# Kernel optimization log

Hardware: AMD Instinct MI355X
Metric: run time of the kernel (lower is better)

## Reference

```python
import jax, jax.numpy as jnp
import numpy as np

INPUT_DIM = 1024
OUTPUT_DIM = 1024
DEGREE = 8


def pentanacci_basis(x, degree):
    # x: [B, I] (already sigmoided). Returns [B, I, degree+1].
    # P0 = 0, P1 = 1, P2 = x, P3 = x, P4 = x^2,
    # Pn = x*P(n-1) + P(n-2) + P(n-3) + P(n-4) + P(n-5) for n >= 5
    zeros = jnp.zeros_like(x)
    ones = jnp.ones_like(x)
    seeds = [zeros, ones, x, x, x * x]
    basis = seeds[: degree + 1]
    for n in range(5, degree + 1):
        basis.append(x * basis[n - 1] + basis[n - 2] + basis[n - 3]
                     + basis[n - 4] + basis[n - 5])
    return jnp.stack(basis, axis=-1)


def setup_inputs() -> dict:
    key = jax.random.key(0)
    kx, kw = jax.random.split(key)
    x = jax.random.normal(kx, (4096, INPUT_DIM), dtype=jnp.float32)
    std = 1.0 / (INPUT_DIM * (DEGREE + 1))
    coeffs = std * jax.random.normal(kw, (INPUT_DIM, OUTPUT_DIM, DEGREE + 1),
                                     dtype=jnp.float32)
    return {"x": x, "coeffs": coeffs}


def reference(x, coeffs):
    degree = coeffs.shape[-1] - 1
    xs = jax.nn.sigmoid(x)                      # [B, I]
    basis = pentanacci_basis(xs, degree)        # [B, I, D+1]
    y = jnp.einsum('bid,iod->bo', basis, coeffs)  # [B, O]
    return y
```

## Files before the change

### kernel.cpp

```cpp
#include <hip/hip_runtime.h>
#include <stdint.h>

#define M_DIM 4096
#define I_DIM 1024
#define O_DIM 1024
#define KB 6
#define K_DIM (I_DIM * KB)
#define SPLITS 4

typedef __attribute__((ext_vector_type(8))) short short8;
typedef __attribute__((ext_vector_type(4))) float f32x4;
typedef __attribute__((ext_vector_type(4))) unsigned int u32x4;
typedef __attribute__((ext_vector_type(4))) float hfloat4;
typedef __attribute__((ext_vector_type(8))) _Float16 h16x8;

__device__ __forceinline__ unsigned short f2bf(float f) {
  union { float f; unsigned int u; } v; v.f = f;
  unsigned int u = v.u;
  unsigned int r = (u + 0x7FFFu + ((u >> 16) & 1u)) >> 16;
  return (unsigned short)r;
}

__global__ __launch_bounds__(256) void k_prep(const float* __restrict__ x,
                                              const float* __restrict__ C,
                                              unsigned short* __restrict__ A,
                                              unsigned short* __restrict__ Bt,
                                              float* __restrict__ partB) {
  const int bid = blockIdx.x;
  if (bid < 2048) {
    int t = bid * 256 + threadIdx.x;
    long e0 = (long)t * 8;
    const hfloat4* xp = (const hfloat4*)(x + e0);
    hfloat4 v0 = xp[0], v1 = xp[1];
    float xv[8];
    xv[0]=v0[0]; xv[1]=v0[1]; xv[2]=v0[2]; xv[3]=v0[3];
    xv[4]=v1[0]; xv[5]=v1[1]; xv[6]=v1[2]; xv[7]=v1[3];
    unsigned short outv[48];
#pragma unroll
    for (int e = 0; e < 8; ++e) {
      float s  = 1.0f / (1.0f + __expf(-xv[e]));
      float b2 = s, b3 = s, b4 = s * s;
      float b5 = fmaf(s, b4, b3 + b2 + 1.0f);
      float b6 = fmaf(s, b5, b4 + b3 + b2 + 1.0f);
      float b7 = fmaf(s, b6, b5 + b4 + b3 + b2);
      float b8 = fmaf(s, b7, b6 + b5 + b4 + b3);
      outv[e*6+0] = f2bf(s);
      outv[e*6+1] = f2bf(b4);
      outv[e*6+2] = f2bf(b5);
      outv[e*6+3] = f2bf(b6);
      outv[e*6+4] = f2bf(b7);
      outv[e*6+5] = f2bf(b8);
    }
    u32x4* dst = (u32x4*)(A + e0 * KB);
    const u32x4* srcv = (const u32x4*)outv;
#pragma unroll
    for (int q = 0; q < 6; ++q) dst[q] = srcv[q];
  } else {
    __shared__ unsigned short tile[32 * 192];
    __shared__ float bred[256];
    int b = bid - 2048;
    int i0 = (b & 31) * 32, o0 = (b >> 5) * 32;
    int t = threadIdx.x;
    int ol = t & 31, ig = t >> 5;
    float bsum = 0.f;
#pragma unroll
    for (int r = 0; r < 4; ++r) {
      int il = ig + r * 8;
      const float* p = C + (size_t)(i0 + il) * (O_DIM * 9) + (size_t)(o0 + ol) * 9;
      float c1 = p[1];
      float c2 = p[2], c3 = p[3], c4 = p[4], c5 = p[5], c6 = p[6], c7 = p[7], c8 = p[8];
      bsum += c1;
      unsigned short* q = &tile[ol * 192 + il * 6];
      q[0] = f2bf(c2 + c3);
      q[1] = f2bf(c4);
      q[2] = f2bf(c5);
      q[3] = f2bf(c6);
      q[4] = f2bf(c7);
      q[5] = f2bf(c8);
    }
    bred[t] = bsum;
    __syncthreads();
    if (t < 32) {
      float s = 0.f;
#pragma unroll
      for (int g = 0; g < 8; ++g) s += bred[g * 32 + t];
      partB[(size_t)(b & 31) * O_DIM + o0 + t] = s;
    }
    const u32x4* lsrc = (const u32x4*)tile;
#pragma unroll
    for (int r = 0; r < 3; ++r) {
      int c = t + r * 256;
      int row = c / 24, off = c % 24;
      u32x4* gdst = (u32x4*)(Bt + (size_t)(o0 + row) * K_DIM + (size_t)i0 * 6 + off * 8);
      *gdst = lsrc[c];
    }
  }
}

__global__ __launch_bounds__(256) void k_bias2(const float* __restrict__ partB,
                                               float* __restrict__ bias) {
  int o = blockIdx.x * 256 + threadIdx.x;
  float s = 0.f;
#pragma unroll
  for (int ib = 0; ib < 32; ++ib) s += partB[(size_t)ib * O_DIM + o];
  bias[o] = s;
}

#define SBAR __builtin_amdgcn_sched_barrier(0)

template<bool SPLIT>
__global__ __launch_bounds__(512, 2) void k_gemm8(const unsigned short* __restrict__ A,
                                                  const unsigned short* __restrict__ B,
                                                  const float* __restrict__ bias,
                                                  void* __restrict__ dst) {
  constexpr int CK = SPLIT ? (K_DIM / SPLITS) : K_DIM;
  constexpr int NT = CK / 64;
  constexpr int PPX = SPLIT ? 8 : 2;
  __shared__ char lds[131072];
  const int tid = threadIdx.x;
  const int lane = tid & 63, wid = tid >> 6;
  const int wm = wid >> 2, wn = wid & 3;
  const int l15 = lane & 15, lk = lane >> 4, l7 = lane & 7;
  const int flat = blockIdx.x + (blockIdx.y << 2) + (blockIdx.z << 6);
  const int xcd = flat & 7, slot = flat >> 3;
  const int panel = xcd * PPX + (slot >> 2);
  const int xn = slot & 3;
  const int ym = panel & 15, zk = panel >> 4;
  const int m0 = ym * 256, n0 = xn * 256;
  const size_t kb = (size_t)zk * CK;
  const int srow = tid >> 3;
  const int cg8 = (((tid & 7) ^ ((tid >> 3) & 7)) * 8);
  const int cx0 = (lk ^ l7) * 16;
  const int cx1 = ((4 + lk) ^ l7) * 16;
  const int arow = wm * 128 + l15;
  const int brow = wn * 64 + l15;

  auto gload = [&](const unsigned short* s, int ldsoff) {
    __builtin_amdgcn_global_load_lds((const __attribute__((address_space(1))) void*)s,
        (__attribute__((address_space(3))) void*)(lds + ldsoff), 16, 0, 0);
  };
  auto stageA = [&](int buf, int h, int kt2) {
    const unsigned short* s = A + (size_t)(m0 + h * 128 + srow) * K_DIM + kb + (size_t)kt2 * 64 + cg8;
    int d = buf * 65536 + h * 16384 + tid * 16;
    gload(s, d);
    gload(s + (size_t)64 * K_DIM, d + 8192);
  };
  auto stageB = [&](int buf, int h, int kt2) {
    const unsigned short* s = B + (size_t)(n0 + h * 128 + srow) * K_DIM + kb + (size_t)kt2 * 64 + cg8;
    int d = buf * 65536 + 32768 + h * 16384 + tid * 16;
    gload(s, d);
    gload(s + (size_t)64 * K_DIM, d + 8192);
  };

  short8 a0[8], b0v[4], a1[8], b1v[4];
  f32x4 acc[8][4];
#pragma unroll
  for (int i = 0; i < 8; ++i)
#pragma unroll
    for (int n = 0; n < 4; ++n)
#pragma unroll
      for (int j = 0; j < 4; ++j) acc[i][n][j] = 0.f;

  auto readK = [&](int buf, int cx, short8 (&av)[8], short8 (&bv)[4]) {
#pragma unroll
    for (int mi = 0; mi < 8; ++mi)
      av[mi] = *(const short8*)(lds + buf * 65536 + (arow + mi * 16) * 128 + cx);
#pragma unroll
    for (int ni = 0; ni < 4; ++ni)
      bv[ni] = *(const short8*)(lds + buf * 65536 + 32768 + (brow + ni * 16) * 128 + cx);
  };
  auto quadK = [&](short8 (&av)[8], short8 (&bv)[4]) {
#pragma unroll
    for (int mi = 0; mi < 8; ++mi)
#pragma unroll
      for (int ni = 0; ni < 4; ++ni)
        acc[mi][ni] = __builtin_amdgcn_mfma_f32_16x16x32_bf16(av[mi], bv[ni], acc[mi][ni], 0, 0, 0);
  };

  stageA(0, 0, 0); stageA(0, 1, 0); stageB(0, 0, 0); stageB(0, 1, 0);
  asm volatile("s_waitcnt vmcnt(0)" ::: "memory"); SBAR;
  __builtin_amdgcn_s_barrier(); SBAR;
  readK(0, cx0, a0, b0v);

#pragma unroll 1
  for (int kt = 0; kt < NT; ++kt) {
    const int buf = kt & 1, nb = buf ^ 1;
    if (kt + 1 < NT) {
      stageA(nb, 0, kt + 1); stageA(nb, 1, kt + 1);
      stageB(nb, 0, kt + 1); stageB(nb, 1, kt + 1);
    }
    readK(buf, cx1, a1, b1v);
    __builtin_amdgcn_s_setprio(1);
    quadK(a0, b0v);
    __builtin_amdgcn_s_setprio(0); SBAR;
    asm volatile("s_waitcnt lgkmcnt(0)" ::: "memory"); SBAR;
    if (kt + 1 < NT) {
      asm volatile("s_waitcnt vmcnt(0)" ::: "memory"); SBAR;
      __builtin_amdgcn_s_barrier(); SBAR;
      readK(nb, cx0, a0, b0v);
    }
    __builtin_amdgcn_s_setprio(1);
    quadK(a1, b1v);
    __builtin_amdgcn_s_setprio(0); SBAR;
  }

  if (SPLIT) {
    _Float16* base = (_Float16*)dst + (size_t)zk * ((size_t)M_DIM * O_DIM);
#pragma unroll
    for (int mi = 0; mi < 8; ++mi) {
      int r0 = m0 + wm * 128 + mi * 16 + (lk << 2);
#pragma unroll
      for (int ni = 0; ni < 4; ++ni) {
        int col = n0 + wn * 64 + ni * 16 + l15;
#pragma unroll
        for (int j = 0; j < 4; ++j)
          base[(size_t)(r0 + j) * O_DIM + col] = (_Float16)acc[mi][ni][j];
      }
    }
  } else {
    float* base = (float*)dst;
#pragma unroll
    for (int mi = 0; mi < 8; ++mi) {
      int r0 = m0 + wm * 128 + mi * 16 + (lk << 2);
#pragma unroll
      for (int ni = 0; ni < 4; ++ni) {
        int col = n0 + wn * 64 + ni * 16 + l15;
        float bv = bias[col];
#pragma unroll
        for (int j = 0; j < 4; ++j)
          base[(size_t)(r0 + j) * O_DIM + col] = acc[mi][ni][j] + bv;
      }
    }
  }
}

__global__ __launch_bounds__(256) void k_reduce(const _Float16* __restrict__ part,
                                                const float* __restrict__ bias,
                                                float* __restrict__ out) {
  size_t t = (size_t)blockIdx.x * 256 + threadIdx.x;
  size_t idx = t * 8;
  const size_t P = (size_t)M_DIM * O_DIM;
  h16x8 s0 = *(const h16x8*)(part + idx);
  h16x8 s1 = *(const h16x8*)(part + P + idx);
  h16x8 s2 = *(const h16x8*)(part + 2 * P + idx);
  h16x8 s3 = *(const h16x8*)(part + 3 * P + idx);
  size_t bo = idx & (O_DIM - 1);
  f32x4 b0 = *(const f32x4*)(bias + bo);
  f32x4 b1 = *(const f32x4*)(bias + bo + 4);
  f32x4 r0, r1;
#pragma unroll
  for (int j = 0; j < 4; ++j) {
    r0[j] = (((float)s0[j] + (float)s1[j]) + ((float)s2[j] + (float)s3[j])) + b0[j];
    r1[j] = (((float)s0[j+4] + (float)s1[j+4]) + ((float)s2[j+4] + (float)s3[j+4])) + b1[j];
  }
  *(f32x4*)(out + idx) = r0;
  *(f32x4*)(out + idx + 4) = r1;
}

extern "C" void kernel_launch(void* const* d_in, const int* in_sizes, int n_in,
                              void* d_out, int out_size, void* d_ws, size_t ws_size,
                              hipStream_t stream) {
  const float* x      = (const float*)d_in[0];
  const float* coeffs = (const float*)d_in[1];
  float* out = (float*)d_out;
  char* ws = (char*)d_ws;
  const size_t offA     = 0;
  const size_t offB     = 50331648;
  const size_t offBias  = offB + 12582912;
  const size_t offPartB = offBias + 4096;
  const size_t offPart  = offPartB + 131072;
  const size_t needSplit = offPart + (size_t)SPLITS * M_DIM * O_DIM * 2;

  unsigned short* A  = (unsigned short*)(ws + offA);
  unsigned short* Bt = (unsigned short*)(ws + offB);
  float* bias        = (float*)(ws + offBias);
  float* partB       = (float*)(ws + offPartB);
  _Float16* part     = (_Float16*)(ws + offPart);

  k_prep<<<3072, 256, 0, stream>>>(x, coeffs, A, Bt, partB);
  k_bias2<<<4, 256, 0, stream>>>(partB, bias);

  if (ws_size >= needSplit) {
    k_gemm8<true><<<dim3(O_DIM / 256, M_DIM / 256, SPLITS), 512, 0, stream>>>(A, Bt, bias, (void*)part);
    k_reduce<<<(M_DIM * O_DIM) / (256 * 8), 256, 0, stream>>>(part, bias, out);
  } else {
    k_gemm8<false><<<dim3(O_DIM / 256, M_DIM / 256, 1), 512, 0, stream>>>(A, Bt, bias, (void*)out);
  }
}
```

Measured before the change: 86.94 us.

## Fuse split-K reduction into GEMM via per-tile atomic counters; reorder MFMA issue

Removes the separate k_reduce launch. The last split-K block to finish each output tile, detected with an atomic counter, sums the four fp16 partials plus bias and writes fp32 output. The counters are zeroed in k_bias2. The main loop also moves the second quadK ahead of the barrier and LDS wait, which changes how MFMA work overlaps with the next LDS reads and may reduce latency hiding. The fused reduction adds a serialized tail to the winning blocks.

```diff
diff --git a/kernel.cpp b/kernel.cpp
--- a/kernel.cpp
+++ b/kernel.cpp
@@ -98,8 +98,10 @@
 }
 
 __global__ __launch_bounds__(256) void k_bias2(const float* __restrict__ partB,
-                                               float* __restrict__ bias) {
+                                               float* __restrict__ bias,
+                                               unsigned int* __restrict__ cnt) {
   int o = blockIdx.x * 256 + threadIdx.x;
+  if (blockIdx.x == 0 && threadIdx.x < 64) cnt[threadIdx.x] = 0;
   float s = 0.f;
 #pragma unroll
   for (int ib = 0; ib < 32; ++ib) s += partB[(size_t)ib * O_DIM + o];
@@ -112,11 +114,14 @@
 __global__ __launch_bounds__(512, 2) void k_gemm8(const unsigned short* __restrict__ A,
                                                   const unsigned short* __restrict__ B,
                                                   const float* __restrict__ bias,
-                                                  void* __restrict__ dst) {
+                                                  _Float16* __restrict__ part,
+                                                  float* __restrict__ out,
+                                                  unsigned int* __restrict__ cnt) {
   constexpr int CK = SPLIT ? (K_DIM / SPLITS) : K_DIM;
   constexpr int NT = CK / 64;
   constexpr int PPX = SPLIT ? 8 : 2;
   __shared__ char lds[131072];
+  __shared__ unsigned int winner;
   const int tid = threadIdx.x;
   const int lane = tid & 63, wid = tid >> 6;
   const int wm = wid >> 2, wn = wid & 3;
@@ -192,6 +197,7 @@
     readK(buf, cx1, a1, b1v);
     __builtin_amdgcn_s_setprio(1);
     quadK(a0, b0v);
+    quadK(a1, b1v);
     __builtin_amdgcn_s_setprio(0); SBAR;
     asm volatile("s_waitcnt lgkmcnt(0)" ::: "memory"); SBAR;
     if (kt + 1 < NT) {
@@ -199,13 +205,10 @@
       __builtin_amdgcn_s_barrier(); SBAR;
       readK(nb, cx0, a0, b0v);
     }
-    __builtin_amdgcn_s_setprio(1);
-    quadK(a1, b1v);
-    __builtin_amdgcn_s_setprio(0); SBAR;
   }
 
   if (SPLIT) {
-    _Float16* base = (_Float16*)dst + (size_t)zk * ((size_t)M_DIM * O_DIM);
+    _Float16* base = part + (size_t)zk * ((size_t)M_DIM * O_DIM);
 #pragma unroll
     for (int mi = 0; mi < 8; ++mi) {
       int r0 = m0 + wm * 128 + mi * 16 + (lk << 2);
@@ -217,8 +220,38 @@
           base[(size_t)(r0 + j) * O_DIM + col] = (_Float16)acc[mi][ni][j];
       }
     }
+    __threadfence();
+    if (tid == 0) {
+      unsigned int old = __hip_atomic_fetch_add(&cnt[ym * 4 + xn], 1u,
+                                                __ATOMIC_ACQ_REL, __HIP_MEMORY_SCOPE_AGENT);
+      winner = (old == SPLITS - 1) ? 1u : 0u;
+    }
+    __syncthreads();
+    if (winner) {
+      __threadfence();
+      const size_t P = (size_t)M_DIM * O_DIM;
+      int rg = tid >> 5, cc = tid & 31;
+      int col = n0 + cc * 8;
+      f32x4 bv0 = *(const f32x4*)(bias + col);
+      f32x4 bv1 = *(const f32x4*)(bias + col + 4);
+#pragma unroll
+      for (int q = 0; q < 16; ++q) {
+        size_t off = (size_t)(m0 + rg * 16 + q) * O_DIM + col;
+        h16x8 p0 = *(const h16x8*)(part + off);
+        h16x8 p1 = *(const h16x8*)(part + P + off);
+        h16x8 p2 = *(const h16x8*)(part + 2 * P + off);
+        h16x8 p3 = *(const h16x8*)(part + 3 * P + off);
+        f32x4 r0, r1;
+#pragma unroll
+        for (int j = 0; j < 4; ++j) {
+          r0[j] = (((float)p0[j] + (float)p1[j]) + ((float)p2[j] + (float)p3[j])) + bv0[j];
+          r1[j] = (((float)p0[j+4] + (float)p1[j+4]) + ((float)p2[j+4] + (float)p3[j+4])) + bv1[j];
+        }
+        *(f32x4*)(out + off) = r0;
+        *(f32x4*)(out + off + 4) = r1;
+      }
+    }
   } else {
-    float* base = (float*)dst;
 #pragma unroll
     for (int mi = 0; mi < 8; ++mi) {
       int r0 = m0 + wm * 128 + mi * 16 + (lk << 2);
@@ -228,33 +261,10 @@
         float bv = bias[col];
 #pragma unroll
         for (int j = 0; j < 4; ++j)
-          base[(size_t)(r0 + j) * O_DIM + col] = acc[mi][ni][j] + bv;
+          out[(size_t)(r0 + j) * O_DIM + col] = acc[mi][ni][j] + bv;
       }
     }
   }
-}
-
-__global__ __launch_bounds__(256) void k_reduce(const _Float16* __restrict__ part,
-                                                const float* __restrict__ bias,
-                                                float* __restrict__ out) {
-  size_t t = (size_t)blockIdx.x * 256 + threadIdx.x;
-  size_t idx = t * 8;
-  const size_t P = (size_t)M_DIM * O_DIM;
-  h16x8 s0 = *(const h16x8*)(part + idx);
-  h16x8 s1 = *(const h16x8*)(part + P + idx);
-  h16x8 s2 = *(const h16x8*)(part + 2 * P + idx);
-  h16x8 s3 = *(const h16x8*)(part + 3 * P + idx);
-  size_t bo = idx & (O_DIM - 1);
-  f32x4 b0 = *(const f32x4*)(bias + bo);
-  f32x4 b1 = *(const f32x4*)(bias + bo + 4);
-  f32x4 r0, r1;
-#pragma unroll
-  for (int j = 0; j < 4; ++j) {
-    r0[j] = (((float)s0[j] + (float)s1[j]) + ((float)s2[j] + (float)s3[j])) + b0[j];
-    r1[j] = (((float)s0[j+4] + (float)s1[j+4]) + ((float)s2[j+4] + (float)s3[j+4])) + b1[j];
-  }
-  *(f32x4*)(out + idx) = r0;
-  *(f32x4*)(out + idx + 4) = r1;
 }
 
 extern "C" void kernel_launch(void* const* d_in, const int* in_sizes, int n_in,
@@ -269,21 +279,22 @@
   const size_t offBias  = offB + 12582912;
   const size_t offPartB = offBias + 4096;
   const size_t offPart  = offPartB + 131072;
-  const size_t needSplit = offPart + (size_t)SPLITS * M_DIM * O_DIM * 2;
+  const size_t offCnt   = offPart + (size_t)SPLITS * M_DIM * O_DIM * 2;
+  const size_t needSplit = offCnt + 256;
 
   unsigned short* A  = (unsigned short*)(ws + offA);
   unsigned short* Bt = (unsigned short*)(ws + offB);
   float* bias        = (float*)(ws + offBias);
   float* partB       = (float*)(ws + offPartB);
   _Float16* part     = (_Float16*)(ws + offPart);
+  unsigned int* cnt  = (unsigned int*)(ws + offCnt);
 
   k_prep<<<3072, 256, 0, stream>>>(x, coeffs, A, Bt, partB);
-  k_bias2<<<4, 256, 0, stream>>>(partB, bias);
+  k_bias2<<<4, 256, 0, stream>>>(partB, bias, cnt);
 
   if (ws_size >= needSplit) {
-    k_gemm8<true><<<dim3(O_DIM / 256, M_DIM / 256, SPLITS), 512, 0, stream>>>(A, Bt, bias, (void*)part);
-    k_reduce<<<(M_DIM * O_DIM) / (256 * 8), 256, 0, stream>>>(part, bias, out);
+    k_gemm8<true><<<dim3(O_DIM / 256, M_DIM / 256, SPLITS), 512, 0, stream>>>(A, Bt, bias, part, out, cnt);
   } else {
-    k_gemm8<false><<<dim3(O_DIM / 256, M_DIM / 256, 1), 512, 0, stream>>>(A, Bt, bias, (void*)out);
+    k_gemm8<false><<<dim3(O_DIM / 256, M_DIM / 256, 1), 512, 0, stream>>>(A, Bt, bias, part, out, cnt);
   }
 }
```

After: 192.1 us. +120.9%, slower.

## Halve GEMM K-tile to 32 and LDS to 64KB, add split-K 8 path

Applied to the files above, without the earlier changes.

The GEMM now stages K-tiles of 32 instead of 64, which halves LDS to 64KB. The double-buffer schedule is restructured around a two-step unrolled loop with new swizzles. Split-K goes from 4 to 8 when workspace allows, giving 512 blocks instead of 256 for better CU fill. The cost is more barriers per unit of work, more fp16 partial-sum traffic into a reduce kernel that now reads 8 planes, and the partB scratch now aliases the partial buffer.

```diff
diff --git a/kernel.cpp b/kernel.cpp
--- a/kernel.cpp
+++ b/kernel.cpp
@@ -6,7 +6,6 @@
 #define O_DIM 1024
 #define KB 6
 #define K_DIM (I_DIM * KB)
-#define SPLITS 4
 
 typedef __attribute__((ext_vector_type(8))) short short8;
 typedef __attribute__((ext_vector_type(4))) float f32x4;
@@ -108,19 +107,20 @@
 
 #define SBAR __builtin_amdgcn_sched_barrier(0)
 
-template<bool SPLIT>
+template<int NSPLIT>
 __global__ __launch_bounds__(512, 2) void k_gemm8(const unsigned short* __restrict__ A,
                                                   const unsigned short* __restrict__ B,
                                                   const float* __restrict__ bias,
-                                                  void* __restrict__ dst) {
-  constexpr int CK = SPLIT ? (K_DIM / SPLITS) : K_DIM;
-  constexpr int NT = CK / 64;
-  constexpr int PPX = SPLIT ? 8 : 2;
-  __shared__ char lds[131072];
+                                                  _Float16* __restrict__ part,
+                                                  float* __restrict__ out) {
+  constexpr int CK = K_DIM / NSPLIT;
+  constexpr int NT = CK / 32;
+  constexpr int PPX = 2 * NSPLIT;
+  __shared__ char lds[65536];
   const int tid = threadIdx.x;
   const int lane = tid & 63, wid = tid >> 6;
   const int wm = wid >> 2, wn = wid & 3;
-  const int l15 = lane & 15, lk = lane >> 4, l7 = lane & 7;
+  const int l15 = lane & 15, lk = lane >> 4;
   const int flat = blockIdx.x + (blockIdx.y << 2) + (blockIdx.z << 6);
   const int xcd = flat & 7, slot = flat >> 3;
   const int panel = xcd * PPX + (slot >> 2);
@@ -128,10 +128,9 @@
   const int ym = panel & 15, zk = panel >> 4;
   const int m0 = ym * 256, n0 = xn * 256;
   const size_t kb = (size_t)zk * CK;
-  const int srow = tid >> 3;
-  const int cg8 = (((tid & 7) ^ ((tid >> 3) & 7)) * 8);
-  const int cx0 = (lk ^ l7) * 16;
-  const int cx1 = ((4 + lk) ^ l7) * 16;
+  const int srow = tid >> 2;
+  const int cg8 = (((tid & 3) ^ ((tid >> 3) & 3)) * 8);
+  const int cx = (lk ^ ((l15 >> 1) & 3)) * 16;
   const int arow = wm * 128 + l15;
   const int brow = wn * 64 + l15;
 
@@ -139,20 +138,17 @@
     __builtin_amdgcn_global_load_lds((const __attribute__((address_space(1))) void*)s,
         (__attribute__((address_space(3))) void*)(lds + ldsoff), 16, 0, 0);
   };
-  auto stageA = [&](int buf, int h, int kt2) {
-    const unsigned short* s = A + (size_t)(m0 + h * 128 + srow) * K_DIM + kb + (size_t)kt2 * 64 + cg8;
-    int d = buf * 65536 + h * 16384 + tid * 16;
-    gload(s, d);
-    gload(s + (size_t)64 * K_DIM, d + 8192);
-  };
-  auto stageB = [&](int buf, int h, int kt2) {
-    const unsigned short* s = B + (size_t)(n0 + h * 128 + srow) * K_DIM + kb + (size_t)kt2 * 64 + cg8;
-    int d = buf * 65536 + 32768 + h * 16384 + tid * 16;
-    gload(s, d);
-    gload(s + (size_t)64 * K_DIM, d + 8192);
-  };
-
-  short8 a0[8], b0v[4], a1[8], b1v[4];
+  auto stageAB = [&](int buf, int kt2) {
+    const unsigned short* sa = A + (size_t)(m0 + srow) * K_DIM + kb + (size_t)kt2 * 32 + cg8;
+    const unsigned short* sb = B + (size_t)(n0 + srow) * K_DIM + kb + (size_t)kt2 * 32 + cg8;
+    int d = buf * 32768 + tid * 16;
+    gload(sa, d);
+    gload(sa + (size_t)128 * K_DIM, d + 8192);
+    gload(sb, d + 16384);
+    gload(sb + (size_t)128 * K_DIM, d + 24576);
+  };
+
+  short8 aA[8], bA[4], aB[8], bB[4];
   f32x4 acc[8][4];
 #pragma unroll
   for (int i = 0; i < 8; ++i)
@@ -161,13 +157,13 @@
 #pragma unroll
       for (int j = 0; j < 4; ++j) acc[i][n][j] = 0.f;
 
-  auto readK = [&](int buf, int cx, short8 (&av)[8], short8 (&bv)[4]) {
+  auto readK = [&](int buf, short8 (&av)[8], short8 (&bv)[4]) {
 #pragma unroll
     for (int mi = 0; mi < 8; ++mi)
-      av[mi] = *(const short8*)(lds + buf * 65536 + (arow + mi * 16) * 128 + cx);
+      av[mi] = *(const short8*)(lds + buf * 32768 + (arow + mi * 16) * 64 + cx);
 #pragma unroll
     for (int ni = 0; ni < 4; ++ni)
-      bv[ni] = *(const short8*)(lds + buf * 65536 + 32768 + (brow + ni * 16) * 128 + cx);
+      bv[ni] = *(const short8*)(lds + buf * 32768 + 16384 + (brow + ni * 16) * 64 + cx);
   };
   auto quadK = [&](short8 (&av)[8], short8 (&bv)[4]) {
 #pragma unroll
@@ -177,35 +173,33 @@
         acc[mi][ni] = __builtin_amdgcn_mfma_f32_16x16x32_bf16(av[mi], bv[ni], acc[mi][ni], 0, 0, 0);
   };
 
-  stageA(0, 0, 0); stageA(0, 1, 0); stageB(0, 0, 0); stageB(0, 1, 0);
+  stageAB(0, 0);
   asm volatile("s_waitcnt vmcnt(0)" ::: "memory"); SBAR;
   __builtin_amdgcn_s_barrier(); SBAR;
-  readK(0, cx0, a0, b0v);
+  readK(0, aA, bA);
 
 #pragma unroll 1
-  for (int kt = 0; kt < NT; ++kt) {
-    const int buf = kt & 1, nb = buf ^ 1;
-    if (kt + 1 < NT) {
-      stageA(nb, 0, kt + 1); stageA(nb, 1, kt + 1);
-      stageB(nb, 0, kt + 1); stageB(nb, 1, kt + 1);
-    }
-    readK(buf, cx1, a1, b1v);
+  for (int kt = 0; kt < NT; kt += 2) {
+    stageAB(1, kt + 1);
     __builtin_amdgcn_s_setprio(1);
-    quadK(a0, b0v);
+    quadK(aA, bA);
     __builtin_amdgcn_s_setprio(0); SBAR;
-    asm volatile("s_waitcnt lgkmcnt(0)" ::: "memory"); SBAR;
-    if (kt + 1 < NT) {
+    asm volatile("s_waitcnt vmcnt(0)" ::: "memory"); SBAR;
+    __builtin_amdgcn_s_barrier(); SBAR;
+    if (kt + 2 < NT) stageAB(0, kt + 2);
+    readK(1, aB, bB);
+    __builtin_amdgcn_s_setprio(1);
+    quadK(aB, bB);
+    __builtin_amdgcn_s_setprio(0); SBAR;
+    if (kt + 2 < NT) {
       asm volatile("s_waitcnt vmcnt(0)" ::: "memory"); SBAR;
       __builtin_amdgcn_s_barrier(); SBAR;
-      readK(nb, cx0, a0, b0v);
-    }
-    __builtin_amdgcn_s_setprio(1);
-    quadK(a1, b1v);
-    __builtin_amdgcn_s_setprio(0); SBAR;
-  }
-
-  if (SPLIT) {
-    _Float16* base = (_Float16*)dst + (size_t)zk * ((size_t)M_DIM * O_DIM);
+      readK(0, aA, bA);
+    }
+  }
+
+  if (NSPLIT > 1) {
+    _Float16* base = part + (size_t)zk * ((size_t)M_DIM * O_DIM);
 #pragma unroll
     for (int mi = 0; mi < 8; ++mi) {
       int r0 = m0 + wm * 128 + mi * 16 + (lk << 2);
@@ -218,7 +212,6 @@
       }
     }
   } else {
-    float* base = (float*)dst;
 #pragma unroll
     for (int mi = 0; mi < 8; ++mi) {
       int r0 = m0 + wm * 128 + mi * 16 + (lk << 2);
@@ -228,31 +221,34 @@
         float bv = bias[col];
 #pragma unroll
         for (int j = 0; j < 4; ++j)
-          base[(size_t)(r0 + j) * O_DIM + col] = acc[mi][ni][j] + bv;
+          out[(size_t)(r0 + j) * O_DIM + col] = acc[mi][ni][j] + bv;
       }
     }
   }
 }
 
+template<int NSPLIT>
 __global__ __launch_bounds__(256) void k_reduce(const _Float16* __restrict__ part,
                                                 const float* __restrict__ bias,
                                                 float* __restrict__ out) {
   size_t t = (size_t)blockIdx.x * 256 + threadIdx.x;
   size_t idx = t * 8;
   const size_t P = (size_t)M_DIM * O_DIM;
-  h16x8 s0 = *(const h16x8*)(part + idx);
-  h16x8 s1 = *(const h16x8*)(part + P + idx);
-  h16x8 s2 = *(const h16x8*)(part + 2 * P + idx);
-  h16x8 s3 = *(const h16x8*)(part + 3 * P + idx);
+  float r[8];
   size_t bo = idx & (O_DIM - 1);
   f32x4 b0 = *(const f32x4*)(bias + bo);
   f32x4 b1 = *(const f32x4*)(bias + bo + 4);
+#pragma unroll
+  for (int j = 0; j < 4; ++j) { r[j] = b0[j]; r[j + 4] = b1[j]; }
+#pragma unroll
+  for (int p = 0; p < NSPLIT; ++p) {
+    h16x8 s = *(const h16x8*)(part + (size_t)p * P + idx);
+#pragma unroll
+    for (int j = 0; j < 8; ++j) r[j] += (float)s[j];
+  }
   f32x4 r0, r1;
 #pragma unroll
-  for (int j = 0; j < 4; ++j) {
-    r0[j] = (((float)s0[j] + (float)s1[j]) + ((float)s2[j] + (float)s3[j])) + b0[j];
-    r1[j] = (((float)s0[j+4] + (float)s1[j+4]) + ((float)s2[j+4] + (float)s3[j+4])) + b1[j];
-  }
+  for (int j = 0; j < 4; ++j) { r0[j] = r[j]; r1[j] = r[j + 4]; }
   *(f32x4*)(out + idx) = r0;
   *(f32x4*)(out + idx + 4) = r1;
 }
@@ -267,9 +263,11 @@
   const size_t offA     = 0;
   const size_t offB     = 50331648;
   const size_t offBias  = offB + 12582912;
-  const size_t offPartB = offBias + 4096;
-  const size_t offPart  = offPartB + 131072;
-  const size_t needSplit = offPart + (size_t)SPLITS * M_DIM * O_DIM * 2;
+  const size_t offPart  = offBias + 4096;
+  const size_t offPartB = offPart;
+  const size_t planeB   = (size_t)M_DIM * O_DIM * 2;
+  const size_t need8 = offPart + 8 * planeB;
+  const size_t need4 = offPart + 4 * planeB;
 
   unsigned short* A  = (unsigned short*)(ws + offA);
   unsigned short* Bt = (unsigned short*)(ws + offB);
@@ -280,10 +278,13 @@
   k_prep<<<3072, 256, 0, stream>>>(x, coeffs, A, Bt, partB);
   k_bias2<<<4, 256, 0, stream>>>(partB, bias);
 
-  if (ws_size >= needSplit) {
-    k_gemm8<true><<<dim3(O_DIM / 256, M_DIM / 256, SPLITS), 512, 0, stream>>>(A, Bt, bias, (void*)part);
-    k_reduce<<<(M_DIM * O_DIM) / (256 * 8), 256, 0, stream>>>(part, bias, out);
+  if (ws_size >= need8) {
+    k_gemm8<8><<<dim3(4, 16, 8), 512, 0, stream>>>(A, Bt, bias, part, out);
+    k_reduce<8><<<(M_DIM * O_DIM) / (256 * 8), 256, 0, stream>>>(part, bias, out);
+  } else if (ws_size >= need4) {
+    k_gemm8<4><<<dim3(4, 16, 4), 512, 0, stream>>>(A, Bt, bias, part, out);
+    k_reduce<4><<<(M_DIM * O_DIM) / (256 * 8), 256, 0, stream>>>(part, bias, out);
   } else {
-    k_gemm8<false><<<dim3(O_DIM / 256, M_DIM / 256, 1), 512, 0, stream>>>(A, Bt, bias, (void*)out);
-  }
-}
+    k_gemm8<1><<<dim3(4, 16, 1), 512, 0, stream>>>(A, Bt, bias, part, out);
+  }
+}
```

Measured after the change: 103.7 us. 19.3% more time.

## Use 4-wave 256x256 GEMM blocks with 128x128 per-wave tiles

Applied to the files above, without the earlier changes.

Each 256x256 output tile is now computed by 4 waves of 256 threads instead of 8 waves of 512. Each wave owns a 128x128 sub-tile with 8x8 MFMA accumulators, so it reuses more LDS fragments per MFMA. Staging is merged into one loop of 16 global-to-LDS loads per thread, and both K-halves' MFMAs now run back to back before the barrier. The cost is far higher VGPR/AGPR pressure, with 256 accumulator floats per lane, and fewer waves to hide latency, at one block per CU.

```diff
diff --git a/kernel.cpp b/kernel.cpp
--- a/kernel.cpp
+++ b/kernel.cpp
@@ -109,17 +109,18 @@
 #define SBAR __builtin_amdgcn_sched_barrier(0)
 
 template<bool SPLIT>
-__global__ __launch_bounds__(512, 2) void k_gemm8(const unsigned short* __restrict__ A,
+__global__ __launch_bounds__(256, 1) void k_gemm8(const unsigned short* __restrict__ A,
                                                   const unsigned short* __restrict__ B,
                                                   const float* __restrict__ bias,
-                                                  void* __restrict__ dst) {
+                                                  _Float16* __restrict__ part,
+                                                  float* __restrict__ out) {
   constexpr int CK = SPLIT ? (K_DIM / SPLITS) : K_DIM;
   constexpr int NT = CK / 64;
   constexpr int PPX = SPLIT ? 8 : 2;
   __shared__ char lds[131072];
   const int tid = threadIdx.x;
   const int lane = tid & 63, wid = tid >> 6;
-  const int wm = wid >> 2, wn = wid & 3;
+  const int wm = wid >> 1, wn = wid & 1;
   const int l15 = lane & 15, lk = lane >> 4, l7 = lane & 7;
   const int flat = blockIdx.x + (blockIdx.y << 2) + (blockIdx.z << 6);
   const int xcd = flat & 7, slot = flat >> 3;
@@ -133,51 +134,49 @@
   const int cx0 = (lk ^ l7) * 16;
   const int cx1 = ((4 + lk) ^ l7) * 16;
   const int arow = wm * 128 + l15;
-  const int brow = wn * 64 + l15;
+  const int brow = wn * 128 + l15;
 
   auto gload = [&](const unsigned short* s, int ldsoff) {
     __builtin_amdgcn_global_load_lds((const __attribute__((address_space(1))) void*)s,
         (__attribute__((address_space(3))) void*)(lds + ldsoff), 16, 0, 0);
   };
-  auto stageA = [&](int buf, int h, int kt2) {
-    const unsigned short* s = A + (size_t)(m0 + h * 128 + srow) * K_DIM + kb + (size_t)kt2 * 64 + cg8;
-    int d = buf * 65536 + h * 16384 + tid * 16;
-    gload(s, d);
-    gload(s + (size_t)64 * K_DIM, d + 8192);
-  };
-  auto stageB = [&](int buf, int h, int kt2) {
-    const unsigned short* s = B + (size_t)(n0 + h * 128 + srow) * K_DIM + kb + (size_t)kt2 * 64 + cg8;
-    int d = buf * 65536 + 32768 + h * 16384 + tid * 16;
-    gload(s, d);
-    gload(s + (size_t)64 * K_DIM, d + 8192);
-  };
-
-  short8 a0[8], b0v[4], a1[8], b1v[4];
-  f32x4 acc[8][4];
+  auto stageAB = [&](int buf, int kt2) {
+    const unsigned short* sa = A + (size_t)(m0 + srow) * K_DIM + kb + (size_t)kt2 * 64 + cg8;
+    const unsigned short* sb = B + (size_t)(n0 + srow) * K_DIM + kb + (size_t)kt2 * 64 + cg8;
+    int d = buf * 65536 + tid * 16;
+#pragma unroll
+    for (int g = 0; g < 8; ++g) {
+      gload(sa + (size_t)(32 * g) * K_DIM, d + g * 4096);
+      gload(sb + (size_t)(32 * g) * K_DIM, d + 32768 + g * 4096);
+    }
+  };
+
+  short8 a0[8], b0v[8], a1[8], b1v[8];
+  f32x4 acc[8][8];
 #pragma unroll
   for (int i = 0; i < 8; ++i)
 #pragma unroll
-    for (int n = 0; n < 4; ++n)
+    for (int n = 0; n < 8; ++n)
 #pragma unroll
       for (int j = 0; j < 4; ++j) acc[i][n][j] = 0.f;
 
-  auto readK = [&](int buf, int cx, short8 (&av)[8], short8 (&bv)[4]) {
+  auto readK = [&](int buf, int cx, short8 (&av)[8], short8 (&bv)[8]) {
 #pragma unroll
     for (int mi = 0; mi < 8; ++mi)
       av[mi] = *(const short8*)(lds + buf * 65536 + (arow + mi * 16) * 128 + cx);
 #pragma unroll
-    for (int ni = 0; ni < 4; ++ni)
+    for (int ni = 0; ni < 8; ++ni)
       bv[ni] = *(const short8*)(lds + buf * 65536 + 32768 + (brow + ni * 16) * 128 + cx);
   };
-  auto quadK = [&](short8 (&av)[8], short8 (&bv)[4]) {
+  auto quadK = [&](short8 (&av)[8], short8 (&bv)[8]) {
 #pragma unroll
     for (int mi = 0; mi < 8; ++mi)
 #pragma unroll
-      for (int ni = 0; ni < 4; ++ni)
+      for (int ni = 0; ni < 8; ++ni)
         acc[mi][ni] = __builtin_amdgcn_mfma_f32_16x16x32_bf16(av[mi], bv[ni], acc[mi][ni], 0, 0, 0);
   };
 
-  stageA(0, 0, 0); stageA(0, 1, 0); stageB(0, 0, 0); stageB(0, 1, 0);
+  stageAB(0, 0);
   asm volatile("s_waitcnt vmcnt(0)" ::: "memory"); SBAR;
   __builtin_amdgcn_s_barrier(); SBAR;
   readK(0, cx0, a0, b0v);
@@ -185,13 +184,11 @@
 #pragma unroll 1
   for (int kt = 0; kt < NT; ++kt) {
     const int buf = kt & 1, nb = buf ^ 1;
-    if (kt + 1 < NT) {
-      stageA(nb, 0, kt + 1); stageA(nb, 1, kt + 1);
-      stageB(nb, 0, kt + 1); stageB(nb, 1, kt + 1);
-    }
+    if (kt + 1 < NT) stageAB(nb, kt + 1);
     readK(buf, cx1, a1, b1v);
     __builtin_amdgcn_s_setprio(1);
     quadK(a0, b0v);
+    quadK(a1, b1v);
     __builtin_amdgcn_s_setprio(0); SBAR;
     asm volatile("s_waitcnt lgkmcnt(0)" ::: "memory"); SBAR;
     if (kt + 1 < NT) {
@@ -199,36 +196,32 @@
       __builtin_amdgcn_s_barrier(); SBAR;
       readK(nb, cx0, a0, b0v);
     }
-    __builtin_amdgcn_s_setprio(1);
-    quadK(a1, b1v);
-    __builtin_amdgcn_s_setprio(0); SBAR;
   }
 
   if (SPLIT) {
-    _Float16* base = (_Float16*)dst + (size_t)zk * ((size_t)M_DIM * O_DIM);
+    _Float16* base = part + (size_t)zk * ((size_t)M_DIM * O_DIM);
 #pragma unroll
     for (int mi = 0; mi < 8; ++mi) {
       int r0 = m0 + wm * 128 + mi * 16 + (lk << 2);
 #pragma unroll
-      for (int ni = 0; ni < 4; ++ni) {
-        int col = n0 + wn * 64 + ni * 16 + l15;
+      for (int ni = 0; ni < 8; ++ni) {
+        int col = n0 + wn * 128 + ni * 16 + l15;
 #pragma unroll
         for (int j = 0; j < 4; ++j)
           base[(size_t)(r0 + j) * O_DIM + col] = (_Float16)acc[mi][ni][j];
       }
     }
   } else {
-    float* base = (float*)dst;
 #pragma unroll
     for (int mi = 0; mi < 8; ++mi) {
       int r0 = m0 + wm * 128 + mi * 16 + (lk << 2);
 #pragma unroll
-      for (int ni = 0; ni < 4; ++ni) {
-        int col = n0 + wn * 64 + ni * 16 + l15;
+      for (int ni = 0; ni < 8; ++ni) {
+        int col = n0 + wn * 128 + ni * 16 + l15;
         float bv = bias[col];
 #pragma unroll
         for (int j = 0; j < 4; ++j)
-          base[(size_t)(r0 + j) * O_DIM + col] = acc[mi][ni][j] + bv;
+          out[(size_t)(r0 + j) * O_DIM + col] = acc[mi][ni][j] + bv;
       }
     }
   }
@@ -281,9 +274,9 @@
   k_bias2<<<4, 256, 0, stream>>>(partB, bias);
 
   if (ws_size >= needSplit) {
-    k_gemm8<true><<<dim3(O_DIM / 256, M_DIM / 256, SPLITS), 512, 0, stream>>>(A, Bt, bias, (void*)part);
+    k_gemm8<true><<<dim3(4, 16, SPLITS), 256, 0, stream>>>(A, Bt, bias, part, out);
     k_reduce<<<(M_DIM * O_DIM) / (256 * 8), 256, 0, stream>>>(part, bias, out);
   } else {
-    k_gemm8<false><<<dim3(O_DIM / 256, M_DIM / 256, 1), 512, 0, stream>>>(A, Bt, bias, (void*)out);
-  }
-}
+    k_gemm8<false><<<dim3(4, 16, 1), 256, 0, stream>>>(A, Bt, bias, part, out);
+  }
+}
```

New measurement: 145.6 us. 1.67x slower.
